# Kernel optimization log

Hardware: AMD Instinct MI355X
Metric: run time of the kernel (lower is better)

The kernel has to match this reference:

```python
import jax, jax.numpy as jnp
import numpy as np

TAU = 2.0  # aggregator_temp


def setup_inputs() -> dict:
    key = jax.random.key(0)
    k1, k2 = jax.random.split(key)
    B, Na, Nv, D = 32, 512, 256, 384
    audio_feats = jax.random.normal(k1, (B, Na, D), dtype=jnp.float32)
    visual_feats = jax.random.normal(k2, (B, Nv, D), dtype=jnp.float32)
    return {"audio_feats": audio_feats, "visual_feats": visual_feats}


def reference(audio_feats, visual_feats):
    # Cross-batch token similarities: (B, B, Na, Nv)
    # token_sims[i, j, n, m] = <audio_feats[i, n], visual_feats[j, m]>
    token_sims = jnp.einsum('ind,jmd->ijnm', audio_feats, visual_feats)
    # logsumexp_pool: tau * logsumexp(sims / tau) over key-token dim (Nv),
    # then mean over query-token dim (Na) -> clip_sims (B, B)
    aggregator = TAU * jax.nn.logsumexp(token_sims / TAU, axis=-1)
    clip_sims = aggregator.mean(axis=-1)
    return clip_sims
```

## Files before the change

### kernel.cpp

```cpp
#include <hip/hip_runtime.h>

constexpr int B_  = 32;
constexpr int Na  = 512;
constexpr int Nv  = 256;
constexpr int D   = 384;

constexpr int BK  = 32;
constexpr int NK  = D / BK;

constexpr int AGROUPS = B_ * 16;
constexpr int BGROUPS = B_ * 8;
constexpr size_t GROUP_BYTES = 12 * 1024;

typedef long  long2v   __attribute__((ext_vector_type(2)));
typedef int   int4v    __attribute__((ext_vector_type(4)));
typedef float floatx16 __attribute__((ext_vector_type(16)));

__global__ void convert_fp8_kernel(const float* __restrict__ a, const float* __restrict__ v,
                                   unsigned char* __restrict__ a8,
                                   unsigned char* __restrict__ b8,
                                   float* __restrict__ out) {
    int gid = blockIdx.x * blockDim.x + threadIdx.x;
    if (gid < B_ * B_) out[gid] = 0.0f;

    const float* src;
    unsigned char* dst;
    int blk = blockIdx.x;
    if (blk < AGROUPS) {
        src = a + (size_t)blk * 32 * D;
        dst = a8 + (size_t)blk * GROUP_BYTES;
    } else {
        int b2 = blk - AGROUPS;
        src = v + (size_t)b2 * 32 * D;
        dst = b8 + (size_t)b2 * GROUP_BYTES;
    }
    const int t = threadIdx.x;
    const int r = t >> 3, q = t & 7;

    #pragma unroll
    for (int p = 0; p < 3; ++p) {
        int k0 = p * 128 + q * 16;
        const float4* s4 = (const float4*)(src + (size_t)r * D + k0);
        float4 f0 = s4[0], f1 = s4[1], f2 = s4[2], f3 = s4[3];
        int w0 = 0, w1 = 0, w2 = 0, w3 = 0;
        w0 = __builtin_amdgcn_cvt_pk_fp8_f32(f0.x, f0.y, w0, false);
        w0 = __builtin_amdgcn_cvt_pk_fp8_f32(f0.z, f0.w, w0, true);
        w1 = __builtin_amdgcn_cvt_pk_fp8_f32(f1.x, f1.y, w1, false);
        w1 = __builtin_amdgcn_cvt_pk_fp8_f32(f1.z, f1.w, w1, true);
        w2 = __builtin_amdgcn_cvt_pk_fp8_f32(f2.x, f2.y, w2, false);
        w2 = __builtin_amdgcn_cvt_pk_fp8_f32(f2.z, f2.w, w2, true);
        w3 = __builtin_amdgcn_cvt_pk_fp8_f32(f3.x, f3.y, w3, false);
        w3 = __builtin_amdgcn_cvt_pk_fp8_f32(f3.z, f3.w, w3, true);
        int kc = k0 >> 5;
        int h2 = (k0 >> 4) & 1;
        int4v o = { w0, w1, w2, w3 };
        *(int4v*)(dst + (size_t)kc * 1024 + h2 * 512 + r * 16) = o;
    }
}

__device__ __forceinline__ float expsum16(floatx16 a) {
    constexpr float INV_TAU_LN2 = 0.7213475204444817f;
    float e[16];
    #pragma unroll
    for (int i = 0; i < 16; ++i) e[i] = exp2f(a[i] * INV_TAU_LN2);
    float t0 = (e[0] + e[1])  + (e[2] + e[3]);
    float t1 = (e[4] + e[5])  + (e[6] + e[7]);
    float t2 = (e[8] + e[9])  + (e[10] + e[11]);
    float t3 = (e[12] + e[13]) + (e[14] + e[15]);
    return (t0 + t1) + (t2 + t3);
}

__global__ __launch_bounds__(256, 2) void gemm_lse_kernel(
        const unsigned char* __restrict__ a8,
        const unsigned char* __restrict__ b8,
        float* __restrict__ out)
{
    const int tid  = threadIdx.x;
    const int lane = tid & 63;
    const int wv   = tid >> 6;

    int b = blockIdx.x;
    const int xcd   = b & 7;      b >>= 3;
    const int bi_lo = b & 3;      b >>= 2;
    const int pr    = b & 1;      b >>= 1;
    const int bj    = b;
    const int bi    = xcd * 4 + bi_lo;
    const int rp    = pr * 4 + wv;

    const size_t laneoff = (size_t)lane * 16;
    const unsigned char* pa0 = a8 + (size_t)(bi * 16 + rp * 2) * GROUP_BYTES + laneoff;
    const unsigned char* pa1 = pa0 + GROUP_BYTES;

    float s0 = 0.0f, s1 = 0.0f;

    #pragma unroll
    for (int ph = 0; ph < 2; ++ph) {
        const unsigned char* pb = b8 + (size_t)(bj * 8 + ph * 4) * GROUP_BYTES + laneoff;

        floatx16 acc[2][4];
        #pragma unroll
        for (int r = 0; r < 2; ++r)
            #pragma unroll
            for (int c = 0; c < 4; ++c)
                acc[r][c] = (floatx16)(0.0f);

        long2v A0 = *(const long2v*)pa0;
        long2v A1 = *(const long2v*)pa1;
        long2v V[4];
        #pragma unroll
        for (int c = 0; c < 4; ++c)
            V[c] = *(const long2v*)(pb + (size_t)c * GROUP_BYTES);

        #pragma unroll
        for (int k = 0; k < NK; ++k) {
            long2v nA0, nA1, nV[4];
            if (k + 1 < NK) {
                const size_t o = (size_t)(k + 1) * 1024;
                nA0 = *(const long2v*)(pa0 + o);
                nA1 = *(const long2v*)(pa1 + o);
                #pragma unroll
                for (int c = 0; c < 4; ++c)
                    nV[c] = *(const long2v*)(pb + (size_t)c * GROUP_BYTES + o);
            }
            __builtin_amdgcn_s_setprio(1);
            #pragma unroll
            for (int c = 0; c < 4; ++c) {
                acc[0][c] = __builtin_amdgcn_mfma_f32_32x32x16_fp8_fp8(V[c].x, A0.x, acc[0][c], 0, 0, 0);
                acc[1][c] = __builtin_amdgcn_mfma_f32_32x32x16_fp8_fp8(V[c].x, A1.x, acc[1][c], 0, 0, 0);
            }
            #pragma unroll
            for (int c = 0; c < 4; ++c) {
                acc[0][c] = __builtin_amdgcn_mfma_f32_32x32x16_fp8_fp8(V[c].y, A0.y, acc[0][c], 0, 0, 0);
                acc[1][c] = __builtin_amdgcn_mfma_f32_32x32x16_fp8_fp8(V[c].y, A1.y, acc[1][c], 0, 0, 0);
            }
            __builtin_amdgcn_s_setprio(0);
            if (k + 1 < NK) {
                A0 = nA0; A1 = nA1;
                #pragma unroll
                for (int c = 0; c < 4; ++c) V[c] = nV[c];
            }
        }

        #pragma unroll
        for (int c = 0; c < 4; ++c) {
            s0 += expsum16(acc[0][c]);
            s1 += expsum16(acc[1][c]);
        }
        __syncthreads();
    }

    s0 += __shfl_xor(s0, 32);
    s1 += __shfl_xor(s1, 32);
    constexpr float TAU_LN2 = 1.3862943611198906f;
    float lse = TAU_LN2 * (log2f(s0) + log2f(s1));
    #pragma unroll
    for (int m = 1; m < 32; m <<= 1) lse += __shfl_xor(lse, m);
    if (lane == 0)
        atomicAdd(&out[bi * 32 + bj], lse * (1.0f / Na));
}

extern "C" void kernel_launch(void* const* d_in, const int* in_sizes, int n_in,
                              void* d_out, int out_size, void* d_ws, size_t ws_size,
                              hipStream_t stream) {
    const float* audio  = (const float*)d_in[0];
    const float* visual = (const float*)d_in[1];
    float* out = (float*)d_out;

    unsigned char* a8 = (unsigned char*)d_ws;
    unsigned char* b8 = a8 + (size_t)AGROUPS * GROUP_BYTES;

    convert_fp8_kernel<<<dim3(AGROUPS + BGROUPS), dim3(256), 0, stream>>>(
        audio, visual, a8, b8, out);
    gemm_lse_kernel<<<dim3(2048), dim3(256), 0, stream>>>(a8, b8, out);
}
```

Baseline: 153.3 us.

## Split visual tokens across waves with LDS reduction and deeper A prefetch

Each block now covers 64 audio rows, and its four waves each take 64 visual tokens. Before, each wave looped over all 256 visual tokens in two phases. The partial exp-sums are combined through shared memory before the log, and the grid grows from 2048 to 8192 blocks. Each wave loads its whole V slice into registers up front and prefetches A three k-steps ahead, aiming for more memory-level parallelism and less serial work per wave. The exp2/log paths switch to fast hardware intrinsics, which costs a little precision and adds a block sync plus extra redundant A loads.

Result: slower. 162.9 us (+6.3%).

```diff
diff --git a/kernel.cpp b/kernel.cpp
--- a/kernel.cpp
+++ b/kernel.cpp
@@ -5,8 +5,7 @@
 constexpr int Nv  = 256;
 constexpr int D   = 384;
 
-constexpr int BK  = 32;
-constexpr int NK  = D / BK;
+constexpr int NK  = D / 32;
 
 constexpr int AGROUPS = B_ * 16;
 constexpr int BGROUPS = B_ * 8;
@@ -62,7 +61,8 @@
     constexpr float INV_TAU_LN2 = 0.7213475204444817f;
     float e[16];
     #pragma unroll
-    for (int i = 0; i < 16; ++i) e[i] = exp2f(a[i] * INV_TAU_LN2);
+    for (int i = 0; i < 16; ++i)
+        e[i] = __builtin_amdgcn_exp2f(a[i] * INV_TAU_LN2);
     float t0 = (e[0] + e[1])  + (e[2] + e[3]);
     float t1 = (e[4] + e[5])  + (e[6] + e[7]);
     float t2 = (e[8] + e[9])  + (e[10] + e[11]);
@@ -75,88 +75,86 @@
         const unsigned char* __restrict__ b8,
         float* __restrict__ out)
 {
+    __shared__ float ms[4][2][32];
+
     const int tid  = threadIdx.x;
     const int lane = tid & 63;
-    const int wv   = tid >> 6;
+    const int vq   = tid >> 6;
 
     int b = blockIdx.x;
     const int xcd   = b & 7;      b >>= 3;
     const int bi_lo = b & 3;      b >>= 2;
-    const int pr    = b & 1;      b >>= 1;
+    const int ro    = b & 7;      b >>= 3;
     const int bj    = b;
     const int bi    = xcd * 4 + bi_lo;
-    const int rp    = pr * 4 + wv;
 
     const size_t laneoff = (size_t)lane * 16;
-    const unsigned char* pa0 = a8 + (size_t)(bi * 16 + rp * 2) * GROUP_BYTES + laneoff;
+    const unsigned char* pa0 = a8 + (size_t)(bi * 16 + ro * 2) * GROUP_BYTES + laneoff;
     const unsigned char* pa1 = pa0 + GROUP_BYTES;
+    const unsigned char* pv0 = b8 + (size_t)(bj * 8 + vq * 2) * GROUP_BYTES + laneoff;
+    const unsigned char* pv1 = pv0 + GROUP_BYTES;
 
-    float s0 = 0.0f, s1 = 0.0f;
+    long2v Apre[4][2];
+    #pragma unroll
+    for (int s = 0; s < 3; ++s) {
+        Apre[s][0] = *(const long2v*)(pa0 + (size_t)s * 1024);
+        Apre[s][1] = *(const long2v*)(pa1 + (size_t)s * 1024);
+    }
+    long2v Vr[2][NK];
+    #pragma unroll
+    for (int kc = 0; kc < NK; ++kc) {
+        Vr[0][kc] = *(const long2v*)(pv0 + (size_t)kc * 1024);
+        Vr[1][kc] = *(const long2v*)(pv1 + (size_t)kc * 1024);
+    }
+
+    floatx16 acc[2][2];
+    #pragma unroll
+    for (int r = 0; r < 2; ++r)
+        #pragma unroll
+        for (int g = 0; g < 2; ++g)
+            acc[r][g] = (floatx16)(0.0f);
 
     #pragma unroll
-    for (int ph = 0; ph < 2; ++ph) {
-        const unsigned char* pb = b8 + (size_t)(bj * 8 + ph * 4) * GROUP_BYTES + laneoff;
-
-        floatx16 acc[2][4];
+    for (int k = 0; k < NK; ++k) {
+        if (k + 3 < NK) {
+            Apre[(k + 3) & 3][0] = *(const long2v*)(pa0 + (size_t)(k + 3) * 1024);
+            Apre[(k + 3) & 3][1] = *(const long2v*)(pa1 + (size_t)(k + 3) * 1024);
+        }
+        __builtin_amdgcn_sched_barrier(0);
+        __builtin_amdgcn_s_setprio(1);
         #pragma unroll
-        for (int r = 0; r < 2; ++r)
-            #pragma unroll
-            for (int c = 0; c < 4; ++c)
-                acc[r][c] = (floatx16)(0.0f);
-
-        long2v A0 = *(const long2v*)pa0;
-        long2v A1 = *(const long2v*)pa1;
-        long2v V[4];
+        for (int g = 0; g < 2; ++g) {
+            acc[0][g] = __builtin_amdgcn_mfma_f32_32x32x16_fp8_fp8(Vr[g][k].x, Apre[k & 3][0].x, acc[0][g], 0, 0, 0);
+            acc[1][g] = __builtin_amdgcn_mfma_f32_32x32x16_fp8_fp8(Vr[g][k].x, Apre[k & 3][1].x, acc[1][g], 0, 0, 0);
+        }
         #pragma unroll
-        for (int c = 0; c < 4; ++c)
-            V[c] = *(const long2v*)(pb + (size_t)c * GROUP_BYTES);
-
-        #pragma unroll
-        for (int k = 0; k < NK; ++k) {
-            long2v nA0, nA1, nV[4];
-            if (k + 1 < NK) {
-                const size_t o = (size_t)(k + 1) * 1024;
-                nA0 = *(const long2v*)(pa0 + o);
-                nA1 = *(const long2v*)(pa1 + o);
-                #pragma unroll
-                for (int c = 0; c < 4; ++c)
-                    nV[c] = *(const long2v*)(pb + (size_t)c * GROUP_BYTES + o);
-            }
-            __builtin_amdgcn_s_setprio(1);
-            #pragma unroll
-            for (int c = 0; c < 4; ++c) {
-                acc[0][c] = __builtin_amdgcn_mfma_f32_32x32x16_fp8_fp8(V[c].x, A0.x, acc[0][c], 0, 0, 0);
-                acc[1][c] = __builtin_amdgcn_mfma_f32_32x32x16_fp8_fp8(V[c].x, A1.x, acc[1][c], 0, 0, 0);
-            }
-            #pragma unroll
-            for (int c = 0; c < 4; ++c) {
-                acc[0][c] = __builtin_amdgcn_mfma_f32_32x32x16_fp8_fp8(V[c].y, A0.y, acc[0][c], 0, 0, 0);
-                acc[1][c] = __builtin_amdgcn_mfma_f32_32x32x16_fp8_fp8(V[c].y, A1.y, acc[1][c], 0, 0, 0);
-            }
-            __builtin_amdgcn_s_setprio(0);
-            if (k + 1 < NK) {
-                A0 = nA0; A1 = nA1;
-                #pragma unroll
-                for (int c = 0; c < 4; ++c) V[c] = nV[c];
-            }
+        for (int g = 0; g < 2; ++g) {
+            acc[0][g] = __builtin_amdgcn_mfma_f32_32x32x16_fp8_fp8(Vr[g][k].y, Apre[k & 3][0].y, acc[0][g], 0, 0, 0);
+            acc[1][g] = __builtin_amdgcn_mfma_f32_32x32x16_fp8_fp8(Vr[g][k].y, Apre[k & 3][1].y, acc[1][g], 0, 0, 0);
         }
-
-        #pragma unroll
-        for (int c = 0; c < 4; ++c) {
-            s0 += expsum16(acc[0][c]);
-            s1 += expsum16(acc[1][c]);
-        }
-        __syncthreads();
+        __builtin_amdgcn_s_setprio(0);
     }
 
+    float s0 = expsum16(acc[0][0]) + expsum16(acc[0][1]);
+    float s1 = expsum16(acc[1][0]) + expsum16(acc[1][1]);
     s0 += __shfl_xor(s0, 32);
     s1 += __shfl_xor(s1, 32);
-    constexpr float TAU_LN2 = 1.3862943611198906f;
-    float lse = TAU_LN2 * (log2f(s0) + log2f(s1));
-    #pragma unroll
-    for (int m = 1; m < 32; m <<= 1) lse += __shfl_xor(lse, m);
-    if (lane == 0)
-        atomicAdd(&out[bi * 32 + bj], lse * (1.0f / Na));
+    if (lane < 32) {
+        ms[vq][0][lane] = s0;
+        ms[vq][1][lane] = s1;
+    }
+    __syncthreads();
+
+    if (tid < 64) {
+        const int g = tid >> 5, r = tid & 31;
+        float e = (ms[0][g][r] + ms[1][g][r]) + (ms[2][g][r] + ms[3][g][r]);
+        constexpr float TAU_LN2 = 1.3862943611198906f;
+        float lse = TAU_LN2 * __builtin_amdgcn_logf(e);
+        #pragma unroll
+        for (int m = 1; m < 64; m <<= 1) lse += __shfl_xor(lse, m);
+        if (tid == 0)
+            atomicAdd(&out[bi * 32 + bj], lse * (1.0f / Na));
+    }
 }
 
 extern "C" void kernel_launch(void* const* d_in, const int* in_sizes, int n_in,
@@ -171,5 +169,5 @@
 
     convert_fp8_kernel<<<dim3(AGROUPS + BGROUPS), dim3(256), 0, stream>>>(
         audio, visual, a8, b8, out);
-    gemm_lse_kernel<<<dim3(2048), dim3(256), 0, stream>>>(a8, b8, out);
+    gemm_lse_kernel<<<dim3(8192), dim3(256), 0, stream>>>(a8, b8, out);
 }
```
